# Kernel optimization log

Hardware: AMD Instinct MI355X
Metric: run time of the kernel (lower is better)

Reference implementation:

```python
import jax, jax.numpy as jnp
import numpy as np

# Module config (init_kwargs)
H, W = 256, 384
NUM_LAYERS = 3
ANG = 7
FACTOR = 1.0
A2 = ANG * ANG
N, RANK, C = 2, 4, 3


def _default_flow():
    # identity sampling grid in [-1, 1], shape (H, W, 2), last dim = (x, y)
    xv, yv = jnp.meshgrid(jnp.linspace(-1.0, 1.0, W), jnp.linspace(-1.0, 1.0, H))
    return jnp.stack([xv, yv], axis=-1).astype(jnp.float32)


def _shifts():
    # per-view constant flow offsets, shape (A2, 2); ordering: outer k (y), inner l (x)
    factor_h = FACTOR * (-1.0 / H)
    factor_w = FACTOR * (-1.0 / W)
    idx = np.arange(-ANG // 2 + 1, ANG // 2 + 1)
    kk, ll = np.meshgrid(idx, idx, indexing='ij')
    return jnp.asarray(np.stack([factor_w * ll.ravel(), factor_h * kk.ravel()], axis=-1),
                       dtype=jnp.float32)


def _grid_sample_border(img, grid):
    # img: (N, C, H, W); grid: (N, A, H, W, 2) in [-1,1], align_corners=True,
    # bilinear, padding_mode='border' (clamp float coord). Returns (N, C, A, H, W).
    n, c, h, w = img.shape
    x = jnp.clip((grid[..., 0] + 1.0) * 0.5 * (w - 1), 0.0, w - 1)
    y = jnp.clip((grid[..., 1] + 1.0) * 0.5 * (h - 1), 0.0, h - 1)
    x0f, y0f = jnp.floor(x), jnp.floor(y)
    x0 = x0f.astype(jnp.int32)
    y0 = y0f.astype(jnp.int32)
    x1 = jnp.minimum(x0 + 1, w - 1)
    y1 = jnp.minimum(y0 + 1, h - 1)
    wx = (x - x0f)[:, None]  # (N, 1, A, H, W)
    wy = (y - y0f)[:, None]

    def gather(im, yy, xx):  # im (C,H,W), yy/xx (A,H,W) -> (C,A,H,W)
        return im[:, yy, xx]

    g = jax.vmap(gather)
    v00 = g(img, y0, x0)
    v01 = g(img, y0, x1)
    v10 = g(img, y1, x0)
    v11 = g(img, y1, x1)
    return (v00 * (1 - wx) * (1 - wy) + v01 * wx * (1 - wy)
            + v10 * (1 - wx) * wy + v11 * wx * wy)


def setup_inputs() -> dict:
    key = jax.random.key(0)
    k1, k2 = jax.random.split(key)
    low_rank = jax.random.normal(k1, (N, NUM_LAYERS, RANK, C, H, W), dtype=jnp.float32)
    planes = jax.random.uniform(k2, (N, NUM_LAYERS), dtype=jnp.float32)
    return {"low_rank": low_rank, "planes": planes}


def reference(low_rank, planes):
    n, num_layers, rank, c, h, w = low_rank.shape
    default = _default_flow()            # (H, W, 2)
    shifts = _shifts()                   # (A2, 2)
    acc = jnp.ones((n, rank * c, A2, h, w), dtype=low_rank.dtype)
    for l in range(num_layers):
        # per-(batch, view) affine grid: default + planes[n,l] * shift[a]
        grid = default[None, None] + planes[:, l][:, None, None, None, None] * shifts[None, :, None, None, :]
        sampled = _grid_sample_border(low_rank[:, l].reshape(n, rank * c, h, w), grid)
        acc = acc * sampled              # multiplicative layer composition
    lf = acc.reshape(n, rank, c, A2, h, w).mean(1)   # mean over rank -> (N, C, A2, H, W)
    return jnp.transpose(lf, (0, 2, 1, 3, 4))        # (N, A2, C, H, W)
```

## Files before the change

kernel.cpp:

```cpp
#include <hip/hip_runtime.h>

#define HH 256
#define WW 384
#define HWSZ (HH*WW)
#define NL 3
#define ANGN 7
#define A2N 49
#define NBATCH 2
#define RANKN 4
#define CN 3
#define RCN (RANKN*CN)

#define WP 392
#define CHS (HH*WP)
#define NCH (NBATCH*NL*RCN)
#define QPR (WP/4)

#define WPX 8
#define GX (WW/WPX)
#define PBN ((HH*GX)/256)

__global__ __launch_bounds__(256) void multilayer_kernel(
    const float* __restrict__ low_rank,
    const float* __restrict__ planes,
    float* __restrict__ out)
{
    int b = blockIdx.x;
    int pb = b % (HWSZ / 256);
    int na = b / (HWSZ / 256);
    int a  = na % A2N;
    int n  = na / A2N;

    int tid = pb * 256 + (int)threadIdx.x;
    int y = tid / WW;
    int x = tid % WW;
    float xf = (float)x, yf = (float)y;

    int lidx = a % ANGN - 3;
    int kidx = a / ANGN - 3;
    float sxa = -(float)lidx * (1.0f / WW) * 0.5f * (float)(WW - 1);
    float sya = -(float)kidx * (1.0f / HH) * 0.5f * (float)(HH - 1);

    float acc[RCN];
#pragma unroll
    for (int i = 0; i < RCN; i++) acc[i] = 1.0f;

#pragma unroll
    for (int l = 0; l < NL; l++) {
        float p = planes[n * NL + l];
        float X = fminf(fmaxf(xf + p * sxa, 0.0f), (float)(WW - 1));
        float Y = fminf(fmaxf(yf + p * sya, 0.0f), (float)(HH - 1));
        float x0f = floorf(X), y0f = floorf(Y);
        int x0 = (int)x0f, y0 = (int)y0f;
        int x1 = min(x0 + 1, WW - 1);
        int y1 = min(y0 + 1, HH - 1);
        float wx = X - x0f, wy = Y - y0f;
        float w00 = (1.0f - wx) * (1.0f - wy);
        float w01 = wx * (1.0f - wy);
        float w10 = (1.0f - wx) * wy;
        float w11 = wx * wy;

        const float* img = low_rank + (size_t)((n * NL + l) * RCN) * HWSZ;
        const float* r0 = img + y0 * WW;
        const float* r1 = img + y1 * WW;

#pragma unroll
        for (int rc = 0; rc < RCN; rc++) {
            float v00 = r0[rc * HWSZ + x0];
            float v01 = r0[rc * HWSZ + x1];
            float v10 = r1[rc * HWSZ + x0];
            float v11 = r1[rc * HWSZ + x1];
            float s = v00 * w00 + v01 * w01 + v10 * w10 + v11 * w11;
            acc[rc] *= s;
        }
    }

    int obase = ((n * A2N + a) * CN) * HWSZ + y * WW + x;
#pragma unroll
    for (int c = 0; c < CN; c++) {
        float s = acc[0 * CN + c] + acc[1 * CN + c] + acc[2 * CN + c] + acc[3 * CN + c];
        out[obase + c * HWSZ] = 0.25f * s;
    }
}

__global__ __launch_bounds__(256) void pad_kernel(const float* __restrict__ src,
                                                  float* __restrict__ dst)
{
    int idx = blockIdx.x * 256 + (int)threadIdx.x;
    int row = idx / 49;
    int qp  = idx - row * 49;
    const float* s = src + (size_t)row * WW;
    float4* d = (float4*)dst + (size_t)row * QPR + qp * 2;
    float4 v0, v1;
    if (qp == 0) {
        float t = s[0];
        v0 = make_float4(t, t, t, t);
        v1 = *(const float4*)(s);
    } else if (qp == 48) {
        v0 = *(const float4*)(s + 380);
        float t = s[WW - 1];
        v1 = make_float4(t, t, t, t);
    } else {
        v0 = *(const float4*)(s + (2 * qp - 1) * 4);
        v1 = *(const float4*)(s + (2 * qp) * 4);
    }
    d[0] = v0;
    d[1] = v1;
}

#define LERP1(HL, I, WX) ((HL)[I] + (WX) * ((HL)[(I)+1] - (HL)[I]))
#define PROD_SET(P, HL, K, WX) do {                   \
    P[0] = LERP1(HL, (K)+0, WX); P[1] = LERP1(HL, (K)+1, WX); \
    P[2] = LERP1(HL, (K)+2, WX); P[3] = LERP1(HL, (K)+3, WX); \
    P[4] = LERP1(HL, (K)+4, WX); P[5] = LERP1(HL, (K)+5, WX); \
    P[6] = LERP1(HL, (K)+6, WX); P[7] = LERP1(HL, (K)+7, WX); \
} while (0)
#define PROD_MUL(P, HL, K, WX) do {                   \
    P[0] *= LERP1(HL, (K)+0, WX); P[1] *= LERP1(HL, (K)+1, WX); \
    P[2] *= LERP1(HL, (K)+2, WX); P[3] *= LERP1(HL, (K)+3, WX); \
    P[4] *= LERP1(HL, (K)+4, WX); P[5] *= LERP1(HL, (K)+5, WX); \
    P[6] *= LERP1(HL, (K)+6, WX); P[7] *= LERP1(HL, (K)+7, WX); \
} while (0)
#define ACC_FMA(A, P, HL, K, WX) do {                 \
    A[0] = fmaf(P[0], LERP1(HL, (K)+0, WX), A[0]); \
    A[1] = fmaf(P[1], LERP1(HL, (K)+1, WX), A[1]); \
    A[2] = fmaf(P[2], LERP1(HL, (K)+2, WX), A[2]); \
    A[3] = fmaf(P[3], LERP1(HL, (K)+3, WX), A[3]); \
    A[4] = fmaf(P[4], LERP1(HL, (K)+4, WX), A[4]); \
    A[5] = fmaf(P[5], LERP1(HL, (K)+5, WX), A[5]); \
    A[6] = fmaf(P[6], LERP1(HL, (K)+6, WX), A[6]); \
    A[7] = fmaf(P[7], LERP1(HL, (K)+7, WX), A[7]); \
} while (0)

#define STAGE(HL, L) do {                                                  \
    const float* cb = basen + (size_t)((L) * RCN + r * CN + c) * CHS;      \
    const float4* q0 = (const float4*)(cb + voff0[L]);                     \
    const float4* q1 = (const float4*)(cb + voff1[L]);                     \
    float4 a0 = q0[0], a1 = q0[1], a2 = q0[2], a3 = q0[3];                 \
    float4 b0 = q1[0], b1 = q1[1], b2 = q1[2], b3 = q1[3];                 \
    float w = wy[L];                                                       \
    HL[2]  = a0.z + w * (b0.z - a0.z);  HL[3]  = a0.w + w * (b0.w - a0.w); \
    HL[4]  = a1.x + w * (b1.x - a1.x);  HL[5]  = a1.y + w * (b1.y - a1.y); \
    HL[6]  = a1.z + w * (b1.z - a1.z);  HL[7]  = a1.w + w * (b1.w - a1.w); \
    HL[8]  = a2.x + w * (b2.x - a2.x);  HL[9]  = a2.y + w * (b2.y - a2.y); \
    HL[10] = a2.z + w * (b2.z - a2.z);  HL[11] = a2.w + w * (b2.w - a2.w); \
    HL[12] = a3.x + w * (b3.x - a3.x);  HL[13] = a3.y + w * (b3.y - a3.y); \
} while (0)

#define SWITCH_SET(P, HL, LI, J) do {                                      \
    float wx = wxl[LI][J];                                                 \
    switch (i0l[LI][J]) {                                                  \
        case 2:  PROD_SET(P, HL, 2, wx); break;                            \
        case 3:  PROD_SET(P, HL, 3, wx); break;                            \
        case 4:  PROD_SET(P, HL, 4, wx); break;                            \
        default: PROD_SET(P, HL, 5, wx); break;                            \
    }                                                                      \
} while (0)
#define SWITCH_MUL(P, HL, LI, J) do {                                      \
    float wx = wxl[LI][J];                                                 \
    switch (i0l[LI][J]) {                                                  \
        case 2:  PROD_MUL(P, HL, 2, wx); break;                            \
        case 3:  PROD_MUL(P, HL, 3, wx); break;                            \
        case 4:  PROD_MUL(P, HL, 4, wx); break;                            \
        default: PROD_MUL(P, HL, 5, wx); break;                            \
    }                                                                      \
} while (0)
#define SWITCH_ACC(A, P, HL, LI, J) do {                                   \
    float wx = wxl[LI][J];                                                 \
    switch (i0l[LI][J]) {                                                  \
        case 2:  ACC_FMA(A, P, HL, 2, wx); break;                          \
        case 3:  ACC_FMA(A, P, HL, 3, wx); break;                          \
        case 4:  ACC_FMA(A, P, HL, 4, wx); break;                          \
        default: ACC_FMA(A, P, HL, 5, wx); break;                          \
    }                                                                      \
} while (0)

#define INIT_J(J) do {                                                     \
    acc[J][0] = 0.0f; acc[J][1] = 0.0f; acc[J][2] = 0.0f; acc[J][3] = 0.0f;\
    acc[J][4] = 0.0f; acc[J][5] = 0.0f; acc[J][6] = 0.0f; acc[J][7] = 0.0f;\
} while (0)

#define DO_J(J) do {                                                       \
    float prod[WPX];                                                       \
    SWITCH_SET(prod, h0, 0, J);                                            \
    SWITCH_MUL(prod, h1, 1, J);                                            \
    SWITCH_ACC(acc[J], prod, h2, 2, J);                                    \
} while (0)

#define STORE_J(J) do {                                                    \
    float* op = out + obase + (size_t)((J) * CN) * HWSZ;                   \
    *(float4*)(op)     = make_float4(acc[J][0] * 0.25f, acc[J][1] * 0.25f, \
                                     acc[J][2] * 0.25f, acc[J][3] * 0.25f);\
    *(float4*)(op + 4) = make_float4(acc[J][4] * 0.25f, acc[J][5] * 0.25f, \
                                     acc[J][6] * 0.25f, acc[J][7] * 0.25f);\
} while (0)

__global__ __launch_bounds__(256) void ml9_kernel(const float* __restrict__ padbuf,
                                                  const float* __restrict__ planes,
                                                  float* __restrict__ out)
{
    int bid = (int)blockIdx.x;
    int g   = (bid & 7) * 252 + (bid >> 3);
    int pb  = g % PBN;
    int t   = g / PBN;
    int k   = t % ANGN;
    int nc  = t / ANGN;
    int c   = nc % CN;
    int n   = nc / CN;

    int g8 = pb * 256 + (int)threadIdx.x;
    int xg = g8 % GX;
    int y  = g8 / GX;
    int xb = xg * WPX;

    const float syk = -(float)(k - 3) * (0.5f * (float)(HH - 1) / (float)HH);

    float wy[NL];
    int   voff0[NL], voff1[NL];
    float wxl[NL][ANGN];
    int   i0l[NL][ANGN];

#pragma unroll
    for (int l = 0; l < NL; l++) {
        float p  = planes[n * NL + l];
        float Y  = fminf(fmaxf((float)y + p * syk, 0.0f), (float)(HH - 1));
        float yf = floorf(Y);
        int y0   = (int)yf;
        if (y0 > HH - 2) y0 = HH - 2;
        wy[l]    = Y - (float)y0;
        voff0[l] = y0 * WP + xb;
        voff1[l] = voff0[l] + WP;
#pragma unroll
        for (int j = 0; j < ANGN; j++) {
            float sxj = -(float)(j - 3) * (0.5f * (float)(WW - 1) / (float)WW);
            float dx  = p * sxj;
            float oxf = floorf(dx);
            float wx  = dx - oxf;
            wxl[l][j] = __uint_as_float(__builtin_amdgcn_readfirstlane(__float_as_uint(wx)));
            i0l[l][j] = __builtin_amdgcn_readfirstlane((int)oxf + 4);
        }
    }

    const float* basen = padbuf + (size_t)(n * NL * RCN) * CHS;

    float acc[ANGN][WPX];
    INIT_J(0); INIT_J(1); INIT_J(2); INIT_J(3); INIT_J(4); INIT_J(5); INIT_J(6);

#pragma unroll 1
    for (int r = 0; r < RANKN; r++) {
        float h0[16], h1[16], h2[16];
        STAGE(h0, 0);
        STAGE(h1, 1);
        STAGE(h2, 2);

        DO_J(0); DO_J(1); DO_J(2); DO_J(3); DO_J(4); DO_J(5); DO_J(6);
    }

    size_t obase = ((size_t)((n * A2N + k * ANGN) * CN + c)) * HWSZ
                 + (size_t)y * WW + xb;
    STORE_J(0); STORE_J(1); STORE_J(2); STORE_J(3);
    STORE_J(4); STORE_J(5); STORE_J(6);
}

extern "C" void kernel_launch(void* const* d_in, const int* in_sizes, int n_in,
                              void* d_out, int out_size, void* d_ws, size_t ws_size,
                              hipStream_t stream) {
    const float* low_rank = (const float*)d_in[0];
    const float* planes   = (const float*)d_in[1];
    float* out = (float*)d_out;

    size_t need = (size_t)NCH * CHS * sizeof(float);
    if (d_ws != nullptr && ws_size >= need) {
        float* padbuf = (float*)d_ws;
        int pad_blocks = (NCH * HH * 49) / 256;
        pad_kernel<<<pad_blocks, 256, 0, stream>>>(low_rank, padbuf);
        int ml_blocks = NBATCH * CN * ANGN * PBN;
        ml9_kernel<<<ml_blocks, 256, 0, stream>>>(padbuf, planes, out);
    } else {
        int blocks = NBATCH * A2N * (HWSZ / 256);
        multilayer_kernel<<<blocks, 256, 0, stream>>>(low_rank, planes, out);
    }
}
```

Baseline: 210.4 us.

## Software-pipeline rank loads, scalarize per-layer offsets, use nontemporal output stores

```diff
diff --git a/kernel.cpp b/kernel.cpp
--- a/kernel.cpp
+++ b/kernel.cpp
@@ -19,6 +19,9 @@
 #define WPX 8
 #define GX (WW/WPX)
 #define PBN ((HH*GX)/256)
+
+typedef float f4v __attribute__((ext_vector_type(4)));
+#define NTSTORE4(PTR, V) __builtin_nontemporal_store(*(const f4v*)&(V), (f4v*)(PTR))
 
 __global__ __launch_bounds__(256) void multilayer_kernel(
     const float* __restrict__ low_rank,
@@ -132,24 +135,37 @@
     A[7] = fmaf(P[7], LERP1(HL, (K)+7, WX), A[7]); \
 } while (0)
 
-#define STAGE(HL, L) do {                                                  \
-    const float* cb = basen + (size_t)((L) * RCN + r * CN + c) * CHS;      \
-    const float4* q0 = (const float4*)(cb + voff0[L]);                     \
-    const float4* q1 = (const float4*)(cb + voff1[L]);                     \
-    float4 a0 = q0[0], a1 = q0[1], a2 = q0[2], a3 = q0[3];                 \
-    float4 b0 = q1[0], b1 = q1[1], b2 = q1[2], b3 = q1[3];                 \
-    float w = wy[L];                                                       \
-    HL[2]  = a0.z + w * (b0.z - a0.z);  HL[3]  = a0.w + w * (b0.w - a0.w); \
-    HL[4]  = a1.x + w * (b1.x - a1.x);  HL[5]  = a1.y + w * (b1.y - a1.y); \
-    HL[6]  = a1.z + w * (b1.z - a1.z);  HL[7]  = a1.w + w * (b1.w - a1.w); \
-    HL[8]  = a2.x + w * (b2.x - a2.x);  HL[9]  = a2.y + w * (b2.y - a2.y); \
-    HL[10] = a2.z + w * (b2.z - a2.z);  HL[11] = a2.w + w * (b2.w - a2.w); \
-    HL[12] = a3.x + w * (b3.x - a3.x);  HL[13] = a3.y + w * (b3.y - a3.y); \
+
+#define DECL_A(L) float4 A##L##q00, A##L##q01, A##L##q02, A##L##q03, \
+                         A##L##q10, A##L##q11, A##L##q12, A##L##q13
+
+#define LOAD_A(L, R) do {                                                  \
+    const float* cb = basen + (size_t)((L) * RCN + (R) * CN + c) * CHS;    \
+    const float4* q0 = (const float4*)(cb + voff0x##L);                    \
+    const float4* q1 = (const float4*)(cb + voff1x##L);                    \
+    A##L##q00 = q0[0]; A##L##q01 = q0[1]; A##L##q02 = q0[2]; A##L##q03 = q0[3]; \
+    A##L##q10 = q1[0]; A##L##q11 = q1[1]; A##L##q12 = q1[2]; A##L##q13 = q1[3]; \
+} while (0)
+
+#define STAGE_A(HL, L) do {                                                \
+    float w = wy##L;                                                       \
+    HL[2]  = A##L##q00.z + w * (A##L##q10.z - A##L##q00.z);                \
+    HL[3]  = A##L##q00.w + w * (A##L##q10.w - A##L##q00.w);                \
+    HL[4]  = A##L##q01.x + w * (A##L##q11.x - A##L##q01.x);                \
+    HL[5]  = A##L##q01.y + w * (A##L##q11.y - A##L##q01.y);                \
+    HL[6]  = A##L##q01.z + w * (A##L##q11.z - A##L##q01.z);                \
+    HL[7]  = A##L##q01.w + w * (A##L##q11.w - A##L##q01.w);                \
+    HL[8]  = A##L##q02.x + w * (A##L##q12.x - A##L##q02.x);                \
+    HL[9]  = A##L##q02.y + w * (A##L##q12.y - A##L##q02.y);                \
+    HL[10] = A##L##q02.z + w * (A##L##q12.z - A##L##q02.z);                \
+    HL[11] = A##L##q02.w + w * (A##L##q12.w - A##L##q02.w);                \
+    HL[12] = A##L##q03.x + w * (A##L##q13.x - A##L##q03.x);                \
+    HL[13] = A##L##q03.y + w * (A##L##q13.y - A##L##q03.y);                \
 } while (0)
 
 #define SWITCH_SET(P, HL, LI, J) do {                                      \
-    float wx = wxl[LI][J];                                                 \
-    switch (i0l[LI][J]) {                                                  \
+    float wx = wx_##LI##_##J;                                              \
+    switch (i0_##LI##_##J) {                                               \
         case 2:  PROD_SET(P, HL, 2, wx); break;                            \
         case 3:  PROD_SET(P, HL, 3, wx); break;                            \
         case 4:  PROD_SET(P, HL, 4, wx); break;                            \
@@ -157,8 +173,8 @@
     }                                                                      \
 } while (0)
 #define SWITCH_MUL(P, HL, LI, J) do {                                      \
-    float wx = wxl[LI][J];                                                 \
-    switch (i0l[LI][J]) {                                                  \
+    float wx = wx_##LI##_##J;                                              \
+    switch (i0_##LI##_##J) {                                               \
         case 2:  PROD_MUL(P, HL, 2, wx); break;                            \
         case 3:  PROD_MUL(P, HL, 3, wx); break;                            \
         case 4:  PROD_MUL(P, HL, 4, wx); break;                            \
@@ -166,8 +182,8 @@
     }                                                                      \
 } while (0)
 #define SWITCH_ACC(A, P, HL, LI, J) do {                                   \
-    float wx = wxl[LI][J];                                                 \
-    switch (i0l[LI][J]) {                                                  \
+    float wx = wx_##LI##_##J;                                              \
+    switch (i0_##LI##_##J) {                                               \
         case 2:  ACC_FMA(A, P, HL, 2, wx); break;                          \
         case 3:  ACC_FMA(A, P, HL, 3, wx); break;                          \
         case 4:  ACC_FMA(A, P, HL, 4, wx); break;                          \
@@ -186,18 +202,44 @@
     SWITCH_MUL(prod, h1, 1, J);                                            \
     SWITCH_ACC(acc[J], prod, h2, 2, J);                                    \
 } while (0)
+#define DO_ALL_J() do { DO_J(0); DO_J(1); DO_J(2); DO_J(3); DO_J(4); DO_J(5); DO_J(6); } while (0)
 
 #define STORE_J(J) do {                                                    \
     float* op = out + obase + (size_t)((J) * CN) * HWSZ;                   \
-    *(float4*)(op)     = make_float4(acc[J][0] * 0.25f, acc[J][1] * 0.25f, \
-                                     acc[J][2] * 0.25f, acc[J][3] * 0.25f);\
-    *(float4*)(op + 4) = make_float4(acc[J][4] * 0.25f, acc[J][5] * 0.25f, \
-                                     acc[J][6] * 0.25f, acc[J][7] * 0.25f);\
-} while (0)
-
-__global__ __launch_bounds__(256) void ml9_kernel(const float* __restrict__ padbuf,
-                                                  const float* __restrict__ planes,
-                                                  float* __restrict__ out)
+    float4 v0 = make_float4(acc[J][0] * 0.25f, acc[J][1] * 0.25f,          \
+                            acc[J][2] * 0.25f, acc[J][3] * 0.25f);         \
+    float4 v1 = make_float4(acc[J][4] * 0.25f, acc[J][5] * 0.25f,          \
+                            acc[J][6] * 0.25f, acc[J][7] * 0.25f);         \
+    NTSTORE4(op, v0); NTSTORE4(op + 4, v1);                                \
+} while (0)
+
+#define PRE_X(L, J)                                                        \
+    float wx_##L##_##J; int i0_##L##_##J;                                  \
+    do {                                                                   \
+        float dx  = p##L * (-(float)((J) - 3) * (0.5f * (float)(WW - 1) / (float)WW)); \
+        float oxf = floorf(dx);                                            \
+        wx_##L##_##J = __uint_as_float(__builtin_amdgcn_readfirstlane(__float_as_uint(dx - oxf))); \
+        i0_##L##_##J = __builtin_amdgcn_readfirstlane((int)oxf + 4);       \
+    } while (0)
+
+#define PRE_L(L)                                                           \
+    float p##L = planes[n * NL + (L)];                                     \
+    float wy##L; int voff0x##L, voff1x##L;                                 \
+    do {                                                                   \
+        float Y  = fminf(fmaxf((float)y + p##L * syk, 0.0f), (float)(HH - 1)); \
+        float yf = floorf(Y);                                              \
+        int y0   = (int)yf;                                                \
+        if (y0 > HH - 2) y0 = HH - 2;                                      \
+        wy##L    = Y - (float)y0;                                          \
+        voff0x##L = y0 * WP + xb;                                          \
+        voff1x##L = voff0x##L + WP;                                        \
+    } while (0);                                                           \
+    PRE_X(L, 0); PRE_X(L, 1); PRE_X(L, 2); PRE_X(L, 3);                    \
+    PRE_X(L, 4); PRE_X(L, 5); PRE_X(L, 6)
+
+__global__ __launch_bounds__(256) void ml10_kernel(const float* __restrict__ padbuf,
+                                                   const float* __restrict__ planes,
+                                                   float* __restrict__ out)
 {
     int bid = (int)blockIdx.x;
     int g   = (bid & 7) * 252 + (bid >> 3);
@@ -215,46 +257,32 @@
 
     const float syk = -(float)(k - 3) * (0.5f * (float)(HH - 1) / (float)HH);
 
-    float wy[NL];
-    int   voff0[NL], voff1[NL];
-    float wxl[NL][ANGN];
-    int   i0l[NL][ANGN];
-
-#pragma unroll
-    for (int l = 0; l < NL; l++) {
-        float p  = planes[n * NL + l];
-        float Y  = fminf(fmaxf((float)y + p * syk, 0.0f), (float)(HH - 1));
-        float yf = floorf(Y);
-        int y0   = (int)yf;
-        if (y0 > HH - 2) y0 = HH - 2;
-        wy[l]    = Y - (float)y0;
-        voff0[l] = y0 * WP + xb;
-        voff1[l] = voff0[l] + WP;
-#pragma unroll
-        for (int j = 0; j < ANGN; j++) {
-            float sxj = -(float)(j - 3) * (0.5f * (float)(WW - 1) / (float)WW);
-            float dx  = p * sxj;
-            float oxf = floorf(dx);
-            float wx  = dx - oxf;
-            wxl[l][j] = __uint_as_float(__builtin_amdgcn_readfirstlane(__float_as_uint(wx)));
-            i0l[l][j] = __builtin_amdgcn_readfirstlane((int)oxf + 4);
-        }
-    }
+    PRE_L(0); PRE_L(1); PRE_L(2);
 
     const float* basen = padbuf + (size_t)(n * NL * RCN) * CHS;
 
     float acc[ANGN][WPX];
     INIT_J(0); INIT_J(1); INIT_J(2); INIT_J(3); INIT_J(4); INIT_J(5); INIT_J(6);
 
-#pragma unroll 1
-    for (int r = 0; r < RANKN; r++) {
-        float h0[16], h1[16], h2[16];
-        STAGE(h0, 0);
-        STAGE(h1, 1);
-        STAGE(h2, 2);
-
-        DO_J(0); DO_J(1); DO_J(2); DO_J(3); DO_J(4); DO_J(5); DO_J(6);
-    }
+    DECL_A(0); DECL_A(1); DECL_A(2);
+    float h0[16], h1[16], h2[16];
+
+    LOAD_A(0, 0); LOAD_A(1, 0); LOAD_A(2, 0);
+
+    STAGE_A(h0, 0); STAGE_A(h1, 1); STAGE_A(h2, 2);
+    LOAD_A(0, 1); LOAD_A(1, 1); LOAD_A(2, 1);
+    DO_ALL_J();
+
+    STAGE_A(h0, 0); STAGE_A(h1, 1); STAGE_A(h2, 2);
+    LOAD_A(0, 2); LOAD_A(1, 2); LOAD_A(2, 2);
+    DO_ALL_J();
+
+    STAGE_A(h0, 0); STAGE_A(h1, 1); STAGE_A(h2, 2);
+    LOAD_A(0, 3); LOAD_A(1, 3); LOAD_A(2, 3);
+    DO_ALL_J();
+
+    STAGE_A(h0, 0); STAGE_A(h1, 1); STAGE_A(h2, 2);
+    DO_ALL_J();
 
     size_t obase = ((size_t)((n * A2N + k * ANGN) * CN + c)) * HWSZ
                  + (size_t)y * WW + xb;
@@ -275,7 +303,7 @@
         int pad_blocks = (NCH * HH * 49) / 256;
         pad_kernel<<<pad_blocks, 256, 0, stream>>>(low_rank, padbuf);
         int ml_blocks = NBATCH * CN * ANGN * PBN;
-        ml9_kernel<<<ml_blocks, 256, 0, stream>>>(padbuf, planes, out);
+        ml10_kernel<<<ml_blocks, 256, 0, stream>>>(padbuf, planes, out);
     } else {
         int blocks = NBATCH * A2N * (HWSZ / 256);
         multilayer_kernel<<<blocks, 256, 0, stream>>>(low_rank, planes, out);
```

After: 252.1 us. 19.8% more time.
